# Kernel optimization log

Hardware: AMD Instinct MI355X
Metric: run time of the kernel (lower is better)

## Reference

```python
import jax, jax.numpy as jnp
import numpy as np


def setup_inputs() -> dict:
    key = jax.random.key(0)
    k1, k2, k3, k4 = jax.random.split(key, 4)
    B, Cin, Cout, H, W = 8, 256, 256, 128, 128
    x = jax.random.normal(k1, (B, Cin, H, W), dtype=jnp.float32)
    delta_weight = jax.random.normal(k2, (B, Cout, Cin, 1, 1), dtype=jnp.float32) * 0.02
    dw_weight = jax.random.normal(k3, (Cin, 1, 3, 3), dtype=jnp.float32) * 0.05
    pw_weight = jax.random.normal(k4, (Cout, Cin, 1, 1), dtype=jnp.float32) * 0.05
    return {"x": x, "delta_weight": delta_weight, "dw_weight": dw_weight, "pw_weight": pw_weight}


def reference(x, delta_weight, dw_weight, pw_weight):
    # Depthwise 3x3 conv, padding=1, groups=Cin. Kernel OIHW = (Cin, 1, 3, 3).
    Cin = x.shape[1]
    out = jax.lax.conv_general_dilated(
        x, dw_weight,
        window_strides=(1, 1), padding=((1, 1), (1, 1)),
        dimension_numbers=("NCHW", "OIHW", "NCHW"),
        feature_group_count=Cin,
    )
    # Per-sample pointwise 1x1: w_final[b] = pw_weight + delta_weight[b]; batched GEMM.
    w_final = pw_weight[None, :, :, 0, 0] + delta_weight[:, :, :, 0, 0]  # (B, Cout, Cin)
    out = jnp.einsum("bchw,boc->bohw", out, w_final)
    return out
```

## Files before the change

kernel.cpp:

```cpp
#include <hip/hip_runtime.h>

#define BATCH 8
#define CIN   256
#define COUT  256
#define HH    128
#define WW    128
#define HW    (HH*WW)

typedef __bf16 bf16x8 __attribute__((ext_vector_type(8)));
typedef float  f32x4  __attribute__((ext_vector_type(4)));

__device__ __forceinline__ unsigned short f2bf(float f) {
    unsigned u = __float_as_uint(f);
    unsigned r = (u + 0x7fffu + ((u >> 16) & 1u)) >> 16;
    return (unsigned short)r;
}

__global__ __launch_bounds__(256) void prep_w_kernel(
    const float* __restrict__ delta, const float* __restrict__ pw,
    unsigned short* __restrict__ Wb)
{
    int i = blockIdx.x * 256 + threadIdx.x;
    float4 d = *(const float4*)(delta + (size_t)i * 4);
    int j = (i * 4) & (COUT * CIN - 1);
    float4 p = *(const float4*)(pw + j);
    ushort4 r;
    r.x = f2bf(d.x + p.x);
    r.y = f2bf(d.y + p.y);
    r.z = f2bf(d.z + p.z);
    r.w = f2bf(d.w + p.w);
    *(ushort4*)(Wb + (size_t)i * 4) = r;
}

__global__ __launch_bounds__(256) void dwconv_kernel(
    const float* __restrict__ x, const float* __restrict__ dw,
    unsigned short* __restrict__ Tt)
{
    __shared__ unsigned short tile[128 * 66];
    __shared__ float kw[64 * 9];

    const int h  = blockIdx.x;
    const int cb = blockIdx.y;
    const int b  = blockIdx.z;
    const int tid = threadIdx.x;

    if (tid < 144) {
        float4 v = *(const float4*)(dw + (size_t)cb * 576 + (size_t)tid * 4);
        *(float4*)(kw + tid * 4) = v;
    }
    __syncthreads();

    const int wq = tid & 31;
    const int cs = tid >> 5;
    const int w0 = wq * 4;

    for (int ci = 0; ci < 8; ++ci) {
        const int c = ci * 8 + cs;
        const float* xp = x + ((size_t)(b * CIN + cb * 64 + c)) * HW;
        const float* kc = kw + c * 9;
        float a0 = 0.f, a1 = 0.f, a2 = 0.f, a3 = 0.f;
        #pragma unroll
        for (int dy = 0; dy < 3; ++dy) {
            const int r = h + dy - 1;
            float4 v = {0.f, 0.f, 0.f, 0.f};
            if (r >= 0 && r < HH) v = *(const float4*)(xp + r * WW + w0);
            float lft = __shfl_up(v.w, 1);
            float rgt = __shfl_down(v.x, 1);
            if (wq == 0)  lft = 0.f;
            if (wq == 31) rgt = 0.f;
            const float k0 = kc[dy * 3 + 0], k1 = kc[dy * 3 + 1], k2 = kc[dy * 3 + 2];
            a0 += k0 * lft + k1 * v.x + k2 * v.y;
            a1 += k0 * v.x + k1 * v.y + k2 * v.z;
            a2 += k0 * v.y + k1 * v.z + k2 * v.w;
            a3 += k0 * v.z + k1 * v.w + k2 * rgt;
        }
        const int base = w0 * 66 + c;
        tile[base]       = f2bf(a0);
        tile[base + 66]  = f2bf(a1);
        tile[base + 132] = f2bf(a2);
        tile[base + 198] = f2bf(a3);
    }
    __syncthreads();

    {
        const int cpair = tid & 31;
        const int wg    = tid >> 5;
        const size_t prow = (size_t)b * HW + (size_t)h * WW;
        #pragma unroll
        for (int wi = 0; wi < 16; ++wi) {
            const int w = wg * 16 + wi;
            unsigned v = *(const unsigned*)&tile[w * 66 + cpair * 2];
            *(unsigned*)&Tt[(prow + w) * CIN + cb * 64 + cpair * 2] = v;
        }
    }
}

__global__ __launch_bounds__(256) void gemm_kernel(
    const unsigned short* __restrict__ Wb,
    const unsigned short* __restrict__ Tt,
    float* __restrict__ out)
{
    __shared__ unsigned short lA[128 * 32];
    __shared__ unsigned short lB[128 * 32];

    const int nt = blockIdx.x;
    const int mt = blockIdx.y;
    const int b  = blockIdx.z;
    const int tid = threadIdx.x;

    const unsigned short* Ab = Wb + ((size_t)b * COUT + mt * 128) * CIN;
    const unsigned short* Bb = Tt + ((size_t)b * HW + nt * 128) * CIN;

    const int lane = tid & 63;
    const int wv   = tid >> 6;
    const int wm   = (wv & 1) * 64;
    const int wn   = (wv >> 1) * 64;
    const int q    = lane >> 4;
    const int rrow = lane & 15;

    const int arow = tid >> 2;
    const int acol = (tid & 3) * 8;

    f32x4 acc[4][4] = {};

    for (int k0 = 0; k0 < CIN; k0 += 32) {
        #pragma unroll
        for (int r = 0; r < 2; ++r) {
            const int row = r * 64 + arow;
            const unsigned short* ga = Ab + (size_t)row * CIN + k0 + acol;
            const unsigned short* gb = Bb + (size_t)row * CIN + k0 + acol;
            __builtin_amdgcn_global_load_lds(
                (const __attribute__((address_space(1))) void*)ga,
                (__attribute__((address_space(3))) void*)(lA + (size_t)(r * 256 + tid) * 8),
                16, 0, 0);
            __builtin_amdgcn_global_load_lds(
                (const __attribute__((address_space(1))) void*)gb,
                (__attribute__((address_space(3))) void*)(lB + (size_t)(r * 256 + tid) * 8),
                16, 0, 0);
        }
        __syncthreads();

        bf16x8 af[4], bfv[4];
        #pragma unroll
        for (int i = 0; i < 4; ++i) {
            af[i]  = *(const bf16x8*)&lA[(wm + i * 16 + rrow) * 32 + q * 8];
            bfv[i] = *(const bf16x8*)&lB[(wn + i * 16 + rrow) * 32 + q * 8];
        }
        #pragma unroll
        for (int i = 0; i < 4; ++i)
            #pragma unroll
            for (int j = 0; j < 4; ++j)
                acc[i][j] = __builtin_amdgcn_mfma_f32_16x16x32_bf16(af[i], bfv[j], acc[i][j], 0, 0, 0);
        __syncthreads();
    }

    float* outp = out + ((size_t)b * COUT + mt * 128 + wm) * HW + (size_t)nt * 128 + wn;
    #pragma unroll
    for (int i = 0; i < 4; ++i)
        #pragma unroll
        for (int j = 0; j < 4; ++j)
            #pragma unroll
            for (int rr = 0; rr < 4; ++rr)
                outp[(size_t)(i * 16 + q * 4 + rr) * HW + j * 16 + rrow] = acc[i][j][rr];
}

extern "C" void kernel_launch(void* const* d_in, const int* in_sizes, int n_in,
                              void* d_out, int out_size, void* d_ws, size_t ws_size,
                              hipStream_t stream)
{
    const float* x     = (const float*)d_in[0];
    const float* delta = (const float*)d_in[1];
    const float* dw    = (const float*)d_in[2];
    const float* pw    = (const float*)d_in[3];
    float* out = (float*)d_out;

    unsigned short* Tt = (unsigned short*)d_ws;
    unsigned short* Wb = (unsigned short*)((char*)d_ws + (size_t)BATCH * HW * CIN * 2);

    prep_w_kernel<<<dim3(512), dim3(256), 0, stream>>>(delta, pw, Wb);
    dwconv_kernel<<<dim3(128, 4, 8), dim3(256), 0, stream>>>(x, dw, Tt);
    gemm_kernel<<<dim3(128, 2, 8), dim3(256), 0, stream>>>(Wb, Tt, out);
}
```

Measured before the change: 286.5 us.

## Fuse weight prep into dwconv, remap blocks, and widen GEMM K-tile with swizzle

Merges the weight-prep kernel into the depthwise-conv kernel as extra blocks, which saves one launch. Each conv block now handles 4 rows instead of 1, and block IDs are remapped across XCDs in both kernels. The GEMM K-tile doubles to 64 and uses an XOR swizzle on LDS slots to reduce bank conflicts and halve the number of barriers per K. In exchange the conv kernel has fewer blocks, which could lower occupancy, and the GEMM uses more LDS.

Measured after the change: 311.7 us. 8.8% more time.

```diff
diff --git a/kernel.cpp b/kernel.cpp
--- a/kernel.cpp
+++ b/kernel.cpp
@@ -16,33 +16,41 @@
     return (unsigned short)r;
 }
 
-__global__ __launch_bounds__(256) void prep_w_kernel(
+#define CONV_BLOCKS 1024
+#define PREP_BLOCKS 64
+
+__global__ __launch_bounds__(256) void dwconv_prep_kernel(
+    const float* __restrict__ x, const float* __restrict__ dw,
     const float* __restrict__ delta, const float* __restrict__ pw,
-    unsigned short* __restrict__ Wb)
+    unsigned short* __restrict__ Tt, unsigned short* __restrict__ Wb)
 {
-    int i = blockIdx.x * 256 + threadIdx.x;
-    float4 d = *(const float4*)(delta + (size_t)i * 4);
-    int j = (i * 4) & (COUT * CIN - 1);
-    float4 p = *(const float4*)(pw + j);
-    ushort4 r;
-    r.x = f2bf(d.x + p.x);
-    r.y = f2bf(d.y + p.y);
-    r.z = f2bf(d.z + p.z);
-    r.w = f2bf(d.w + p.w);
-    *(ushort4*)(Wb + (size_t)i * 4) = r;
-}
-
-__global__ __launch_bounds__(256) void dwconv_kernel(
-    const float* __restrict__ x, const float* __restrict__ dw,
-    unsigned short* __restrict__ Tt)
-{
+    const int tid = threadIdx.x;
+
+    if ((int)blockIdx.x >= CONV_BLOCKS) {
+        const int t0 = (((int)blockIdx.x - CONV_BLOCKS) * 256 + tid) * 8;
+        #pragma unroll
+        for (int qq = 0; qq < 8; ++qq) {
+            const int i = t0 + qq;
+            float4 d = *(const float4*)(delta + (size_t)i * 4);
+            const int j = (i * 4) & (COUT * CIN - 1);
+            float4 p = *(const float4*)(pw + j);
+            ushort4 r;
+            r.x = f2bf(d.x + p.x);
+            r.y = f2bf(d.y + p.y);
+            r.z = f2bf(d.z + p.z);
+            r.w = f2bf(d.w + p.w);
+            *(ushort4*)(Wb + (size_t)i * 4) = r;
+        }
+        return;
+    }
+
     __shared__ unsigned short tile[128 * 66];
     __shared__ float kw[64 * 9];
 
-    const int h  = blockIdx.x;
-    const int cb = blockIdx.y;
-    const int b  = blockIdx.z;
-    const int tid = threadIdx.x;
+    const int L  = ((int)blockIdx.x & 7) * (CONV_BLOCKS / 8) + ((int)blockIdx.x >> 3);
+    const int hb = L & 31;
+    const int cb = (L >> 5) & 3;
+    const int b  = L >> 7;
 
     if (tid < 144) {
         float4 v = *(const float4*)(dw + (size_t)cb * 576 + (size_t)tid * 4);
@@ -54,44 +62,49 @@
     const int cs = tid >> 5;
     const int w0 = wq * 4;
 
-    for (int ci = 0; ci < 8; ++ci) {
-        const int c = ci * 8 + cs;
-        const float* xp = x + ((size_t)(b * CIN + cb * 64 + c)) * HW;
-        const float* kc = kw + c * 9;
-        float a0 = 0.f, a1 = 0.f, a2 = 0.f, a3 = 0.f;
-        #pragma unroll
-        for (int dy = 0; dy < 3; ++dy) {
-            const int r = h + dy - 1;
-            float4 v = {0.f, 0.f, 0.f, 0.f};
-            if (r >= 0 && r < HH) v = *(const float4*)(xp + r * WW + w0);
-            float lft = __shfl_up(v.w, 1);
-            float rgt = __shfl_down(v.x, 1);
-            if (wq == 0)  lft = 0.f;
-            if (wq == 31) rgt = 0.f;
-            const float k0 = kc[dy * 3 + 0], k1 = kc[dy * 3 + 1], k2 = kc[dy * 3 + 2];
-            a0 += k0 * lft + k1 * v.x + k2 * v.y;
-            a1 += k0 * v.x + k1 * v.y + k2 * v.z;
-            a2 += k0 * v.y + k1 * v.z + k2 * v.w;
-            a3 += k0 * v.z + k1 * v.w + k2 * rgt;
-        }
-        const int base = w0 * 66 + c;
-        tile[base]       = f2bf(a0);
-        tile[base + 66]  = f2bf(a1);
-        tile[base + 132] = f2bf(a2);
-        tile[base + 198] = f2bf(a3);
-    }
-    __syncthreads();
-
-    {
-        const int cpair = tid & 31;
-        const int wg    = tid >> 5;
-        const size_t prow = (size_t)b * HW + (size_t)h * WW;
-        #pragma unroll
-        for (int wi = 0; wi < 16; ++wi) {
-            const int w = wg * 16 + wi;
-            unsigned v = *(const unsigned*)&tile[w * 66 + cpair * 2];
-            *(unsigned*)&Tt[(prow + w) * CIN + cb * 64 + cpair * 2] = v;
-        }
+    for (int hh = 0; hh < 4; ++hh) {
+        const int h = hb * 4 + hh;
+
+        for (int ci = 0; ci < 8; ++ci) {
+            const int c = ci * 8 + cs;
+            const float* xp = x + ((size_t)(b * CIN + cb * 64 + c)) * HW;
+            const float* kc = kw + c * 9;
+            float a0 = 0.f, a1 = 0.f, a2 = 0.f, a3 = 0.f;
+            #pragma unroll
+            for (int dy = 0; dy < 3; ++dy) {
+                const int r = h + dy - 1;
+                float4 v = {0.f, 0.f, 0.f, 0.f};
+                if (r >= 0 && r < HH) v = *(const float4*)(xp + r * WW + w0);
+                float lft = __shfl_up(v.w, 1);
+                float rgt = __shfl_down(v.x, 1);
+                if (wq == 0)  lft = 0.f;
+                if (wq == 31) rgt = 0.f;
+                const float k0 = kc[dy * 3 + 0], k1 = kc[dy * 3 + 1], k2 = kc[dy * 3 + 2];
+                a0 += k0 * lft + k1 * v.x + k2 * v.y;
+                a1 += k0 * v.x + k1 * v.y + k2 * v.z;
+                a2 += k0 * v.y + k1 * v.z + k2 * v.w;
+                a3 += k0 * v.z + k1 * v.w + k2 * rgt;
+            }
+            const int base = w0 * 66 + c;
+            tile[base]       = f2bf(a0);
+            tile[base + 66]  = f2bf(a1);
+            tile[base + 132] = f2bf(a2);
+            tile[base + 198] = f2bf(a3);
+        }
+        __syncthreads();
+
+        {
+            const int cpair = tid & 31;
+            const int wg    = tid >> 5;
+            const size_t prow = (size_t)b * HW + (size_t)h * WW;
+            #pragma unroll
+            for (int wi = 0; wi < 16; ++wi) {
+                const int w = wg * 16 + wi;
+                unsigned v = *(const unsigned*)&tile[w * 66 + cpair * 2];
+                *(unsigned*)&Tt[(prow + w) * CIN + cb * 64 + cpair * 2] = v;
+            }
+        }
+        __syncthreads();
     }
 }
 
@@ -100,12 +113,13 @@
     const unsigned short* __restrict__ Tt,
     float* __restrict__ out)
 {
-    __shared__ unsigned short lA[128 * 32];
-    __shared__ unsigned short lB[128 * 32];
-
-    const int nt = blockIdx.x;
-    const int mt = blockIdx.y;
-    const int b  = blockIdx.z;
+    __shared__ unsigned short lA[128 * 64];
+    __shared__ unsigned short lB[128 * 64];
+
+    const int L  = ((int)blockIdx.x & 7) * 256 + ((int)blockIdx.x >> 3);
+    const int mt = L & 1;
+    const int nt = (L >> 1) & 127;
+    const int b  = L >> 8;
     const int tid = threadIdx.x;
 
     const unsigned short* Ab = Wb + ((size_t)b * COUT + mt * 128) * CIN;
@@ -118,39 +132,43 @@
     const int q    = lane >> 4;
     const int rrow = lane & 15;
 
-    const int arow = tid >> 2;
-    const int acol = (tid & 3) * 8;
-
     f32x4 acc[4][4] = {};
 
-    for (int k0 = 0; k0 < CIN; k0 += 32) {
-        #pragma unroll
-        for (int r = 0; r < 2; ++r) {
-            const int row = r * 64 + arow;
-            const unsigned short* ga = Ab + (size_t)row * CIN + k0 + acol;
-            const unsigned short* gb = Bb + (size_t)row * CIN + k0 + acol;
+    for (int k0 = 0; k0 < CIN; k0 += 64) {
+        #pragma unroll
+        for (int r = 0; r < 4; ++r) {
+            const int i     = r * 256 + tid;
+            const int row   = i >> 3;
+            const int pslot = i & 7;
+            const int lslot = pslot ^ (row & 7);
+            const unsigned short* ga = Ab + (size_t)row * CIN + k0 + lslot * 8;
+            const unsigned short* gb = Bb + (size_t)row * CIN + k0 + lslot * 8;
             __builtin_amdgcn_global_load_lds(
                 (const __attribute__((address_space(1))) void*)ga,
-                (__attribute__((address_space(3))) void*)(lA + (size_t)(r * 256 + tid) * 8),
+                (__attribute__((address_space(3))) void*)(lA + (size_t)i * 8),
                 16, 0, 0);
             __builtin_amdgcn_global_load_lds(
                 (const __attribute__((address_space(1))) void*)gb,
-                (__attribute__((address_space(3))) void*)(lB + (size_t)(r * 256 + tid) * 8),
+                (__attribute__((address_space(3))) void*)(lB + (size_t)i * 8),
                 16, 0, 0);
         }
         __syncthreads();
 
-        bf16x8 af[4], bfv[4];
-        #pragma unroll
-        for (int i = 0; i < 4; ++i) {
-            af[i]  = *(const bf16x8*)&lA[(wm + i * 16 + rrow) * 32 + q * 8];
-            bfv[i] = *(const bf16x8*)&lB[(wn + i * 16 + rrow) * 32 + q * 8];
-        }
-        #pragma unroll
-        for (int i = 0; i < 4; ++i)
-            #pragma unroll
-            for (int j = 0; j < 4; ++j)
-                acc[i][j] = __builtin_amdgcn_mfma_f32_16x16x32_bf16(af[i], bfv[j], acc[i][j], 0, 0, 0);
+        #pragma unroll
+        for (int kk = 0; kk < 2; ++kk) {
+            bf16x8 af[4], bfv[4];
+            const int slot = (kk * 4 + q) ^ (rrow & 7);
+            #pragma unroll
+            for (int i = 0; i < 4; ++i) {
+                af[i]  = *(const bf16x8*)&lA[(wm + i * 16 + rrow) * 64 + slot * 8];
+                bfv[i] = *(const bf16x8*)&lB[(wn + i * 16 + rrow) * 64 + slot * 8];
+            }
+            #pragma unroll
+            for (int i = 0; i < 4; ++i)
+                #pragma unroll
+                for (int j = 0; j < 4; ++j)
+                    acc[i][j] = __builtin_amdgcn_mfma_f32_16x16x32_bf16(af[i], bfv[j], acc[i][j], 0, 0, 0);
+        }
         __syncthreads();
     }
 
@@ -177,7 +195,7 @@
     unsigned short* Tt = (unsigned short*)d_ws;
     unsigned short* Wb = (unsigned short*)((char*)d_ws + (size_t)BATCH * HW * CIN * 2);
 
-    prep_w_kernel<<<dim3(512), dim3(256), 0, stream>>>(delta, pw, Wb);
-    dwconv_kernel<<<dim3(128, 4, 8), dim3(256), 0, stream>>>(x, dw, Tt);
-    gemm_kernel<<<dim3(128, 2, 8), dim3(256), 0, stream>>>(Wb, Tt, out);
-}
+    dwconv_prep_kernel<<<dim3(CONV_BLOCKS + PREP_BLOCKS), dim3(256), 0, stream>>>(
+        x, dw, delta, pw, Tt, Wb);
+    gemm_kernel<<<dim3(2048), dim3(256), 0, stream>>>(Wb, Tt, out);
+}
```
